# Optimization experiments

Measured on AMD Instinct MI355X. Metric: run time of the kernel, lower is better.

Reference implementation:

```python
import jax, jax.numpy as jnp
import numpy as np

N_NODES = 100000
N_EDGES = 1600000
D_IN = 128
D_H = 128          # hidden_channels * heads (heads=1)
N_LAYERS = 5
N_GRAPHS = 64
N_TARGETS = 1
EPS = 1e-5
NEG_SLOPE = 0.2    # PyG GATConv leaky_relu default


def setup_inputs() -> dict:
    key = jax.random.key(0)
    ks = jax.random.split(key, 16)
    x = jax.random.normal(ks[0], (N_NODES, D_IN), dtype=jnp.float32)
    edge_index = jax.random.randint(ks[1], (2, N_EDGES), 0, N_NODES, dtype=jnp.int32)
    batch = jnp.sort(jax.random.randint(ks[2], (N_NODES,), 0, N_GRAPHS, dtype=jnp.int32))
    s = 1.0 / np.sqrt(D_H)
    W = jax.random.normal(ks[3], (N_LAYERS, D_IN, D_H), dtype=jnp.float32) * s
    a_src = jax.random.normal(ks[4], (N_LAYERS, D_H), dtype=jnp.float32) * s
    a_dst = jax.random.normal(ks[5], (N_LAYERS, D_H), dtype=jnp.float32) * s
    b = jax.random.normal(ks[6], (N_LAYERS, D_H), dtype=jnp.float32) * 0.01
    bn_gamma = jnp.ones((N_LAYERS, D_H), dtype=jnp.float32) + 0.1 * jax.random.normal(ks[7], (N_LAYERS, D_H), dtype=jnp.float32)
    bn_beta = 0.1 * jax.random.normal(ks[8], (N_LAYERS, D_H), dtype=jnp.float32)
    bn_mean = 0.1 * jax.random.normal(ks[9], (N_LAYERS, D_H), dtype=jnp.float32)
    bn_var = jax.random.uniform(ks[10], (N_LAYERS, D_H), dtype=jnp.float32, minval=0.5, maxval=1.5)
    lin_w = jax.random.normal(ks[11], (D_H, N_TARGETS), dtype=jnp.float32) * s
    lin_b = jnp.zeros((N_TARGETS,), dtype=jnp.float32)
    return {"x": x, "edge_index": edge_index, "batch": batch, "W": W,
            "a_src": a_src, "a_dst": a_dst, "b": b,
            "bn_gamma": bn_gamma, "bn_beta": bn_beta, "bn_mean": bn_mean,
            "bn_var": bn_var, "lin_w": lin_w, "lin_b": lin_b}


def _gat_layer(h, src, dst, W, a_s, a_d, bias):
    # PyG GATConv (heads=1): linear transform, per-edge attention, softmax over
    # incoming edges of each destination node, weighted sum aggregation.
    xp = h @ W                                   # [N, C]
    s_node = xp @ a_s                            # [N]
    d_node = xp @ a_d                            # [N]
    e = jax.nn.leaky_relu(s_node[src] + d_node[dst], NEG_SLOPE)   # [E]
    m = jax.ops.segment_max(e, dst, num_segments=N_NODES)         # [N]
    w = jnp.exp(e - m[dst])                                       # [E]
    denom = jax.ops.segment_sum(w, dst, num_segments=N_NODES)     # [N] (>0: self-loops)
    alpha = w / denom[dst]                                        # [E]
    out = jax.ops.segment_sum(alpha[:, None] * xp[src], dst, num_segments=N_NODES)
    return out + bias


def reference(x, edge_index, batch, W, a_src, a_dst, b,
              bn_gamma, bn_beta, bn_mean, bn_var, lin_w, lin_b):
    # add self-loops (PyG GATConv default add_self_loops=True)
    loops = jnp.arange(N_NODES, dtype=edge_index.dtype)
    src = jnp.concatenate([edge_index[0], loops])
    dst = jnp.concatenate([edge_index[1], loops])
    h = x
    for l in range(N_LAYERS):
        h = _gat_layer(h, src, dst, W[l], a_src[l], a_dst[l], b[l])
        h = jax.nn.relu(h)
        # dropout: identity (eval mode); BatchNorm1d in eval mode (running stats)
        h = (h - bn_mean[l]) * (bn_gamma[l] / jnp.sqrt(bn_var[l] + EPS)) + bn_beta[l]
    # global mean pool over graphs
    sums = jax.ops.segment_sum(h, batch, num_segments=N_GRAPHS)            # [G, C]
    cnt = jax.ops.segment_sum(jnp.ones((N_NODES,), h.dtype), batch, num_segments=N_GRAPHS)
    g = sums / jnp.maximum(cnt, 1.0)[:, None]
    return g @ lin_w + lin_b
```

## Files before the change

### kernel.cpp

```cpp
#include <hip/hip_runtime.h>
#include <hip/hip_fp16.h>
#include <math.h>


#define NN 100000
#define NE 1600000
#define DH 128
#define NL 5
#define NG 64

static constexpr int ET = NE + NN;
static constexpr int NBK = (NN + 255) >> 8;
static constexpr int CAP = 6144;
static constexpr int GB0 = (NN + 127) / 128;
static constexpr int SBK = (ET + 4095) / 4096;
static constexpr int PW = (NL * DH * DH) / 256;
static constexpr int PB = (NL * DH + 255) / 256;
static constexpr int PC = (NN + 4095) / 4096;

typedef __attribute__((ext_vector_type(8))) _Float16 f16x8;
typedef __attribute__((ext_vector_type(4))) float f32x4;
typedef __attribute__((ext_vector_type(2))) float f32x2;

__device__ __forceinline__ unsigned short f2h(float v) {
    __half h = __float2half(v);
    return *reinterpret_cast<unsigned short*>(&h);
}
__device__ __forceinline__ float h2f(unsigned short u) {
    __half h = *reinterpret_cast<__half*>(&u);
    return __half2float(h);
}


__global__ __launch_bounds__(256) void k_prep(const float* __restrict__ W,
                                              unsigned short* __restrict__ wtg,
                                              const float* __restrict__ ga,
                                              const float* __restrict__ be,
                                              const float* __restrict__ me,
                                              const float* __restrict__ va,
                                              float* __restrict__ g2,
                                              float* __restrict__ b2,
                                              const int* __restrict__ batch,
                                              int* __restrict__ cnts) {
    __shared__ int hc[NG];
    int bid = blockIdx.x, t = threadIdx.x;
    if (bid < PW) {
        int i = bid * 256 + t;
        int l = i >> 14, rem = i & 16383;
        int k = rem >> 7, c = rem & 127;
        wtg[(l << 14) + (c << 7) + k] = f2h(W[i]);
    } else if (bid < PW + PB) {
        int i = (bid - PW) * 256 + t;
        if (i < NL * DH) {
            float s = ga[i] * rsqrtf(va[i] + 1e-5f);
            g2[i] = s;
            b2[i] = be[i] - me[i] * s;
        }
    } else {
        if (t < NG) hc[t] = 0;
        __syncthreads();
        int base = (bid - PW - PB) * 4096;
#pragma unroll
        for (int k = 0; k < 16; ++k) {
            int i = base + k * 256 + t;
            if (i < NN) atomicAdd(&hc[batch[i]], 1);
        }
        __syncthreads();
        if (t < NG && hc[t]) atomicAdd(&cnts[t], hc[t]);
    }
}


template <bool F32IN>
__device__ __forceinline__ void gemm_body(char* lds, int bid,
                                          const void* __restrict__ Av,
                                          const unsigned short* __restrict__ Wt,
                                          const float* __restrict__ a_s,
                                          const float* __restrict__ a_d,
                                          unsigned char* __restrict__ xq,
                                          float* __restrict__ s_node,
                                          float* __restrict__ d_node) {
    int tid = threadIdx.x;
    int w = tid >> 6, l = tid & 63;
    int row0 = bid * 128;
    {
        int col = tid >> 2, seg = tid & 3;
        const char* srcp = (const char*)Wt + col * 256 + seg * 64;
#pragma unroll
        for (int i = 0; i < 4; ++i) {
            int off = seg * 64 + i * 16;
            *(uint4*)(lds + col * 256 + (off ^ ((col & 7) << 4))) =
                *(const uint4*)(srcp + i * 16);
        }
    }
    int arow = row0 + w * 16 + (l & 15);
    int arc = min(arow, NN - 1);
    f16x8 af[4];
    if constexpr (F32IN) {
        const float* ap = (const float*)Av + (size_t)arc * DH + ((l >> 4) << 3);
#pragma unroll
        for (int ks = 0; ks < 4; ++ks) {
            float4 u0 = *(const float4*)(ap + ks * 32);
            float4 u1 = *(const float4*)(ap + ks * 32 + 4);
            f16x8 v = {(_Float16)u0.x, (_Float16)u0.y, (_Float16)u0.z, (_Float16)u0.w,
                       (_Float16)u1.x, (_Float16)u1.y, (_Float16)u1.z, (_Float16)u1.w};
            af[ks] = v;
        }
    } else {
        const unsigned short* ap =
            (const unsigned short*)Av + (size_t)arc * DH + ((l >> 4) << 3);
#pragma unroll
        for (int ks = 0; ks < 4; ++ks)
            af[ks] = *(const f16x8*)(ap + ks * 32);
    }
    __syncthreads();

    f32x4 acc[8];
#pragma unroll
    for (int ct = 0; ct < 8; ++ct) acc[ct] = (f32x4){0.f, 0.f, 0.f, 0.f};
#pragma unroll
    for (int ct = 0; ct < 8; ++ct) {
        int col = ct * 16 + (l & 15);
        int cb = col * 256;
        int sw = (col & 7) << 4;
#pragma unroll
        for (int ks = 0; ks < 4; ++ks) {
            f16x8 bfr = *(const f16x8*)(lds + cb + ((ks * 64 + ((l >> 4) << 4)) ^ sw));
            acc[ct] = __builtin_amdgcn_mfma_f32_16x16x32_f16(af[ks], bfr, acc[ct], 0, 0, 0);
        }
    }

    float asv[8], adv[8];
#pragma unroll
    for (int ct = 0; ct < 8; ++ct) {
        asv[ct] = a_s[ct * 16 + (l & 15)];
        adv[ct] = a_d[ct * 16 + (l & 15)];
    }
    float ps[4] = {0.f, 0.f, 0.f, 0.f}, pd[4] = {0.f, 0.f, 0.f, 0.f};
#pragma unroll
    for (int ct = 0; ct < 8; ++ct)
#pragma unroll
        for (int r = 0; r < 4; ++r) {
            ps[r] = fmaf(acc[ct][r], asv[ct], ps[r]);
            pd[r] = fmaf(acc[ct][r], adv[ct], pd[r]);
        }
#pragma unroll
    for (int off = 8; off >= 1; off >>= 1)
#pragma unroll
        for (int r = 0; r < 4; ++r) {
            ps[r] += __shfl_xor(ps[r], off, 64);
            pd[r] += __shfl_xor(pd[r], off, 64);
        }
    int rbase = row0 + w * 16 + ((l >> 4) << 2);
    if ((l & 15) == 0) {
#pragma unroll
        for (int r = 0; r < 4; ++r) {
            int row = rbase + r;
            if (row < NN) { s_node[row] = ps[r]; d_node[row] = pd[r]; }
        }
    }
#pragma unroll
    for (int r = 0; r < 4; ++r) {
        int row = rbase + r;
        if (row < NN) {
            unsigned char* op = xq + (size_t)row * DH + (l & 15);
#pragma unroll
            for (int ct = 0; ct < 8; ++ct) {
                int pk = __builtin_amdgcn_cvt_pk_fp8_f32(acc[ct][r], 0.f, 0, false);
                op[ct * 16] = (unsigned char)(pk & 0xff);
            }
        }
    }
}


__device__ __forceinline__ void bscatter_body(char* smem, int bid,
                                              const int* __restrict__ src,
                                              const int* __restrict__ dst,
                                              int* __restrict__ bcnt,
                                              int* __restrict__ pairs) {
    int* lcnt = (int*)smem;
    int* lbase = lcnt + NBK;
    for (int i = threadIdx.x; i < NBK; i += 512) lcnt[i] = 0;
    __syncthreads();
    int base = bid * 4096;
    int es[8], ed[8], er[8];
#pragma unroll
    for (int k = 0; k < 8; ++k) {
        int i = base + k * 512 + threadIdx.x;
        if (i < ET) {
            int s, d;
            if (i < NE) { s = src[i]; d = dst[i]; } else { s = d = i - NE; }
            es[k] = s; ed[k] = d;
            er[k] = atomicAdd(&lcnt[d >> 8], 1);
        } else {
            ed[k] = -1;
        }
    }
    __syncthreads();
    for (int i = threadIdx.x; i < NBK; i += 512)
        lbase[i] = lcnt[i] ? atomicAdd(&bcnt[i], lcnt[i]) : 0;
    __syncthreads();
#pragma unroll
    for (int k = 0; k < 8; ++k) {
        if (ed[k] >= 0) {
            int bk = ed[k] >> 8;
            pairs[(size_t)bk * CAP + lbase[bk] + er[k]] =
                es[k] | ((ed[k] & 255) << 17);
        }
    }
}


__global__ __launch_bounds__(512) void k_mega(const float* __restrict__ x,
                                              const unsigned short* __restrict__ Wt,
                                              const float* __restrict__ a_s,
                                              const float* __restrict__ a_d,
                                              unsigned char* __restrict__ xq,
                                              float* __restrict__ s_node,
                                              float* __restrict__ d_node,
                                              const int* __restrict__ src,
                                              const int* __restrict__ dst,
                                              int* __restrict__ bcnt,
                                              int* __restrict__ pairs) {
    __shared__ __align__(16) char smem[35904];
    if (blockIdx.x < GB0)
        gemm_body<true>(smem, blockIdx.x, x, Wt, a_s, a_d, xq, s_node, d_node);
    else
        bscatter_body(smem, blockIdx.x - GB0, src, dst, bcnt, pairs);
}


__global__ __launch_bounds__(512) void k_gemm(const unsigned short* __restrict__ A,
                                              const unsigned short* __restrict__ Wt,
                                              const float* __restrict__ a_s,
                                              const float* __restrict__ a_d,
                                              unsigned char* __restrict__ xq,
                                              float* __restrict__ s_node,
                                              float* __restrict__ d_node) {
    __shared__ __align__(16) char lds[32768];
    gemm_body<false>(lds, blockIdx.x, A, Wt, a_s, a_d, xq, s_node, d_node);
}


__global__ __launch_bounds__(512) void k_bscan(const int* __restrict__ bcnt,
                                               int* __restrict__ bbase,
                                               int* __restrict__ row_ptr) {
    __shared__ int sm[512];
    int t = threadIdx.x;
    int v = (t < NBK) ? bcnt[t] : 0;
    sm[t] = v;
    __syncthreads();
    for (int off = 1; off < 512; off <<= 1) {
        int u = (t >= off) ? sm[t - off] : 0;
        __syncthreads();
        sm[t] += u;
        __syncthreads();
    }
    if (t < NBK) bbase[t] = sm[t] - v;
    if (t == 0) { bbase[NBK] = ET; row_ptr[NN] = ET; }
}

__global__ __launch_bounds__(256) void k_bfinal(const int* __restrict__ pairs,
                                                const int* __restrict__ bcnt,
                                                const int* __restrict__ bbase,
                                                int* __restrict__ row_ptr,
                                                int* __restrict__ csr_src) {
    __shared__ int ldeg[256];
    __shared__ int lcur[256];
    __shared__ int sm[256];
    int b = blockIdx.x, t = threadIdx.x;
    int n0 = b << 8;
    int e0 = bbase[b];
    int cb = bcnt[b];
    const int* slab = pairs + (size_t)b * CAP;
    ldeg[t] = 0;
    __syncthreads();
    for (int j = t; j < cb; j += 256)
        atomicAdd(&ldeg[(slab[j] >> 17) & 255], 1);
    __syncthreads();
    int v = ldeg[t];
    sm[t] = v;
    __syncthreads();
    for (int off = 1; off < 256; off <<= 1) {
        int u = (t >= off) ? sm[t - off] : 0;
        __syncthreads();
        sm[t] += u;
        __syncthreads();
    }
    int excl = sm[t] - v;
    lcur[t] = excl;
    int n = n0 + t;
    if (n < NN) row_ptr[n] = e0 + excl;
    __syncthreads();
    for (int j = t; j < cb; j += 256) {
        int p = slab[j];
        int local = atomicAdd(&lcur[(p >> 17) & 255], 1);
        csr_src[e0 + local] = p & 0x1FFFF;
    }
}


__global__ __launch_bounds__(256) void k_aggr(const unsigned char* __restrict__ xq,
                                              const float* __restrict__ s_node,
                                              const float* __restrict__ d_node,
                                              const int* __restrict__ row_ptr,
                                              const int* __restrict__ csr_src,
                                              const float* __restrict__ bias,
                                              const float* __restrict__ g2,
                                              const float* __restrict__ b2,
                                              unsigned short* __restrict__ hout) {
    __shared__ float2 stash[4][2][64];
    int wid = threadIdx.x >> 6, lane = threadIdx.x & 63;
    int hi = lane >> 5, cl = lane & 31;
    int n = blockIdx.x * 8 + wid * 2 + hi;
    int s0 = row_ptr[n], s1 = row_ptr[n + 1];
    int deg = s1 - s0;
    float dn = d_node[n];

    int off0 = 0, off1 = 0;
    float e0 = -1e30f, e1 = -1e30f;
    {
        int j0 = s0 + cl;
        if (j0 < s1) {
            int s = csr_src[j0];
            off0 = s << 7;
            float t = s_node[s] + dn;
            e0 = (t >= 0.f) ? t : 0.2f * t;
        }
        int j1 = s0 + 32 + cl;
        if (j1 < s1) {
            int s = csr_src[j1];
            off1 = s << 7;
            float t = s_node[s] + dn;
            e1 = (t >= 0.f) ? t : 0.2f * t;
        }
    }
    float mx = fmaxf(e0, e1);
    for (int j = s0 + 64 + cl; j < s1; j += 32) {
        int s = csr_src[j];
        float t = s_node[s] + dn;
        t = (t >= 0.f) ? t : 0.2f * t;
        mx = fmaxf(mx, t);
    }
#pragma unroll
    for (int off = 16; off >= 1; off >>= 1)
        mx = fmaxf(mx, __shfl_xor(mx, off, 32));

    float w0 = (e0 > -1e29f) ? __expf(e0 - mx) : 0.f;
    float w1 = (e1 > -1e29f) ? __expf(e1 - mx) : 0.f;
    float denom = w0 + w1;
#pragma unroll
    for (int off = 16; off >= 1; off >>= 1)
        denom += __shfl_xor(denom, off, 32);

    stash[wid][hi][cl]      = make_float2(w0, __int_as_float(off0));
    stash[wid][hi][cl + 32] = make_float2(w1, __int_as_float(off1));

    unsigned int cl4 = (unsigned int)cl << 2;
    const char* xbase = (const char*)xq;
    float acc0 = 0.f, acc1 = 0.f, acc2 = 0.f, acc3 = 0.f;
    int cnt = min(deg, 64);
#pragma unroll 8
    for (int t = 0; t < cnt; ++t) {
        float2 p = stash[wid][hi][t];
        float w = p.x;
        unsigned int voff = (unsigned int)__float_as_int(p.y) + cl4;
        unsigned int v = *(const unsigned int*)(xbase + voff);
        f32x2 d0 = __builtin_amdgcn_cvt_pk_f32_fp8(v, false);
        f32x2 d1 = __builtin_amdgcn_cvt_pk_f32_fp8(v, true);
        acc0 = fmaf(w, d0[0], acc0);
        acc1 = fmaf(w, d0[1], acc1);
        acc2 = fmaf(w, d1[0], acc2);
        acc3 = fmaf(w, d1[1], acc3);
    }
    for (int j = s0 + 64; j < s1; ++j) {
        int s = csr_src[j];
        float t = s_node[s] + dn;
        t = (t >= 0.f) ? t : 0.2f * t;
        float w = __expf(t - mx);
        denom += w;
        unsigned int voff = ((unsigned int)s << 7) + cl4;
        unsigned int v = *(const unsigned int*)(xbase + voff);
        f32x2 d0 = __builtin_amdgcn_cvt_pk_f32_fp8(v, false);
        f32x2 d1 = __builtin_amdgcn_cvt_pk_f32_fp8(v, true);
        acc0 = fmaf(w, d0[0], acc0);
        acc1 = fmaf(w, d0[1], acc1);
        acc2 = fmaf(w, d1[0], acc2);
        acc3 = fmaf(w, d1[1], acc3);
    }

    float inv = 1.f / denom;
    int c = cl << 2;
    float4 bi = *(const float4*)(bias + c);
    float4 gg = *(const float4*)(g2 + c);
    float4 bb = *(const float4*)(b2 + c);
    float o0 = fmaxf(fmaf(acc0, inv, bi.x), 0.f) * gg.x + bb.x;
    float o1 = fmaxf(fmaf(acc1, inv, bi.y), 0.f) * gg.y + bb.y;
    float o2 = fmaxf(fmaf(acc2, inv, bi.z), 0.f) * gg.z + bb.z;
    float o3 = fmaxf(fmaf(acc3, inv, bi.w), 0.f) * gg.w + bb.w;
    ushort4 ov = {f2h(o0), f2h(o1), f2h(o2), f2h(o3)};
    *(ushort4*)(hout + (size_t)n * DH + c) = ov;
}


__global__ __launch_bounds__(128) void k_pool1(const unsigned short* __restrict__ h,
                                               const int* __restrict__ batch,
                                               float* __restrict__ sums) {
    int c = threadIdx.x;
    int n0 = blockIdx.x * 64;
    int n1 = min(NN, n0 + 64);
    if (n0 >= NN) return;
    float acc = 0.f;
    int cur = batch[n0];
    for (int n = n0; n < n1; ++n) {
        int g = batch[n];
        if (g != cur) {
            atomicAdd(&sums[cur * DH + c], acc);
            acc = 0.f; cur = g;
        }
        acc += h2f(h[(size_t)n * DH + c]);
    }
    atomicAdd(&sums[cur * DH + c], acc);
}

__global__ __launch_bounds__(128) void k_pool2(const float* __restrict__ sums,
                                               const int* __restrict__ cnts,
                                               const float* __restrict__ lin_w,
                                               const float* __restrict__ lin_b,
                                               float* __restrict__ out) {
    __shared__ float sm[128];
    int g = blockIdx.x, c = threadIdx.x;
    float cnt = fmaxf((float)cnts[g], 1.f);
    sm[c] = (sums[g * DH + c] / cnt) * lin_w[c];
    __syncthreads();
    for (int off = 64; off >= 1; off >>= 1) {
        if (c < off) sm[c] += sm[c + off];
        __syncthreads();
    }
    if (c == 0) out[g] = sm[0] + lin_b[0];
}


extern "C" void kernel_launch(void* const* d_in, const int* in_sizes, int n_in,
                              void* d_out, int out_size, void* d_ws, size_t ws_size,
                              hipStream_t stream) {
    const float* x     = (const float*)d_in[0];
    const int*   ei    = (const int*)d_in[1];
    const int*   batch = (const int*)d_in[2];
    const float* W     = (const float*)d_in[3];
    const float* a_src = (const float*)d_in[4];
    const float* a_dst = (const float*)d_in[5];
    const float* b     = (const float*)d_in[6];
    const float* bn_g  = (const float*)d_in[7];
    const float* bn_b  = (const float*)d_in[8];
    const float* bn_m  = (const float*)d_in[9];
    const float* bn_v  = (const float*)d_in[10];
    const float* lin_w = (const float*)d_in[11];
    const float* lin_b = (const float*)d_in[12];
    float* out = (float*)d_out;

    const int* srcp = ei;
    const int* dstp = ei + NE;

    char* wsp = (char*)d_ws;
    size_t off = 0;
    auto alloc = [&](size_t bytes) -> void* {
        void* p = wsp + off;
        off = (off + bytes + 511) & ~((size_t)511);
        return p;
    };
    unsigned char*  xq  = (unsigned char*)alloc((size_t)NN * DH);
    unsigned short* hb  = (unsigned short*)alloc((size_t)NN * DH * 2);
    unsigned short* wtg = (unsigned short*)alloc((size_t)NL * DH * DH * 2);
    float* g2      = (float*)alloc((size_t)NL * DH * 4);
    float* b2      = (float*)alloc((size_t)NL * DH * 4);
    float* s_node  = (float*)alloc((size_t)NN * 4);
    float* d_node  = (float*)alloc((size_t)NN * 4);
    int*   row_ptr = (int*)alloc((size_t)(NN + 1) * 4);
    int*   csr_src = (int*)alloc((size_t)ET * 4);
    int*   pairs   = (int*)alloc((size_t)NBK * CAP * 4);
    int*   bcnt    = (int*)alloc((size_t)NBK * 4);
    int*   bbase   = (int*)alloc((size_t)(NBK + 1) * 4);
    float* sums    = (float*)alloc((size_t)NG * DH * 4);
    int*   cnts    = (int*)alloc((size_t)NG * 4);

    hipError_t e0_ = hipMemsetAsync(bcnt, 0, (size_t)NBK * 4, stream); (void)e0_;
    hipError_t e1_ = hipMemsetAsync(sums, 0, (size_t)NG * DH * 4, stream); (void)e1_;
    hipError_t e2_ = hipMemsetAsync(cnts, 0, (size_t)NG * 4, stream); (void)e2_;

    k_prep<<<PW + PB + PC, 256, 0, stream>>>(W, wtg, bn_g, bn_b, bn_m, bn_v,
                                             g2, b2, batch, cnts);

    k_mega<<<GB0 + SBK, 512, 0, stream>>>(x, wtg, a_src, a_dst, xq,
                                          s_node, d_node, srcp, dstp, bcnt, pairs);
    k_bscan<<<1, 512, 0, stream>>>(bcnt, bbase, row_ptr);
    k_bfinal<<<NBK, 256, 0, stream>>>(pairs, bcnt, bbase, row_ptr, csr_src);

    for (int l = 0; l < NL; ++l) {
        if (l > 0)
            k_gemm<<<GB0, 512, 0, stream>>>(hb, wtg + (size_t)l * DH * DH,
                                            a_src + l * DH, a_dst + l * DH,
                                            xq, s_node, d_node);
        k_aggr<<<NN / 8, 256, 0, stream>>>(xq, s_node, d_node, row_ptr, csr_src,
                                           b + l * DH, g2 + l * DH, b2 + l * DH,
                                           hb);
    }

    k_pool1<<<(NN + 63) / 64, 128, 0, stream>>>(hb, batch, sums);
    k_pool2<<<NG, 128, 0, stream>>>(sums, cnts, lin_w, lin_b, out);
}
```

Measured before the change: 384.3 us.

## Stage fp8 GEMM output through LDS, fold bucket scan into bfinal, unroll aggregation

```diff
diff --git a/kernel.cpp b/kernel.cpp
--- a/kernel.cpp
+++ b/kernel.cpp
@@ -17,6 +17,7 @@
 static constexpr int PW = (NL * DH * DH) / 256;
 static constexpr int PB = (NL * DH + 255) / 256;
 static constexpr int PC = (NN + 4095) / 4096;
+static constexpr int LROW = 144;
 
 typedef __attribute__((ext_vector_type(8))) _Float16 f16x8;
 typedef __attribute__((ext_vector_type(4))) float f32x4;
@@ -159,16 +160,26 @@
             if (row < NN) { s_node[row] = ps[r]; d_node[row] = pd[r]; }
         }
     }
+
+    __syncthreads();
+    int rl0 = w * 16 + ((l >> 4) << 2);
 #pragma unroll
     for (int r = 0; r < 4; ++r) {
-        int row = rbase + r;
-        if (row < NN) {
-            unsigned char* op = xq + (size_t)row * DH + (l & 15);
-#pragma unroll
-            for (int ct = 0; ct < 8; ++ct) {
-                int pk = __builtin_amdgcn_cvt_pk_fp8_f32(acc[ct][r], 0.f, 0, false);
-                op[ct * 16] = (unsigned char)(pk & 0xff);
-            }
+#pragma unroll
+        for (int ct = 0; ct < 8; ++ct) {
+            int pk = __builtin_amdgcn_cvt_pk_fp8_f32(acc[ct][r], 0.f, 0, false);
+            lds[(rl0 + r) * LROW + ct * 16 + (l & 15)] = (char)(pk & 0xff);
+        }
+    }
+    __syncthreads();
+    size_t base = (size_t)row0 * DH;
+    size_t limit = (size_t)NN * DH;
+#pragma unroll
+    for (int p = 0; p < 2; ++p) {
+        int q = (tid + p * 512) * 16;
+        if (base + q < limit) {
+            int row = q >> 7, col = q & 127;
+            *(uint4*)(xq + base + q) = *(const uint4*)(lds + row * LROW + col);
         }
     }
 }
@@ -223,7 +234,7 @@
                                               const int* __restrict__ dst,
                                               int* __restrict__ bcnt,
                                               int* __restrict__ pairs) {
-    __shared__ __align__(16) char smem[35904];
+    __shared__ __align__(16) char smem[32768];
     if (blockIdx.x < GB0)
         gemm_body<true>(smem, blockIdx.x, x, Wt, a_s, a_d, xq, s_node, d_node);
     else
@@ -243,27 +254,8 @@
 }
 
 
-__global__ __launch_bounds__(512) void k_bscan(const int* __restrict__ bcnt,
-                                               int* __restrict__ bbase,
-                                               int* __restrict__ row_ptr) {
-    __shared__ int sm[512];
-    int t = threadIdx.x;
-    int v = (t < NBK) ? bcnt[t] : 0;
-    sm[t] = v;
-    __syncthreads();
-    for (int off = 1; off < 512; off <<= 1) {
-        int u = (t >= off) ? sm[t - off] : 0;
-        __syncthreads();
-        sm[t] += u;
-        __syncthreads();
-    }
-    if (t < NBK) bbase[t] = sm[t] - v;
-    if (t == 0) { bbase[NBK] = ET; row_ptr[NN] = ET; }
-}
-
 __global__ __launch_bounds__(256) void k_bfinal(const int* __restrict__ pairs,
                                                 const int* __restrict__ bcnt,
-                                                const int* __restrict__ bbase,
                                                 int* __restrict__ row_ptr,
                                                 int* __restrict__ csr_src) {
     __shared__ int ldeg[256];
@@ -271,8 +263,17 @@
     __shared__ int sm[256];
     int b = blockIdx.x, t = threadIdx.x;
     int n0 = b << 8;
-    int e0 = bbase[b];
+    int psum = 0;
+    for (int j = t; j < b; j += 256) psum += bcnt[j];
+    sm[t] = psum;
+    __syncthreads();
+    for (int off = 128; off >= 1; off >>= 1) {
+        if (t < off) sm[t] += sm[t + off];
+        __syncthreads();
+    }
+    int e0 = sm[0];
     int cb = bcnt[b];
+    __syncthreads();
     const int* slab = pairs + (size_t)b * CAP;
     ldeg[t] = 0;
     __syncthreads();
@@ -292,6 +293,7 @@
     lcur[t] = excl;
     int n = n0 + t;
     if (n < NN) row_ptr[n] = e0 + excl;
+    if (b == 0 && t == 0) row_ptr[NN] = ET;
     __syncthreads();
     for (int j = t; j < cb; j += 256) {
         int p = slab[j];
@@ -361,7 +363,7 @@
     const char* xbase = (const char*)xq;
     float acc0 = 0.f, acc1 = 0.f, acc2 = 0.f, acc3 = 0.f;
     int cnt = min(deg, 64);
-#pragma unroll 8
+#pragma unroll 16
     for (int t = 0; t < cnt; ++t) {
         float2 p = stash[wid][hi][t];
         float w = p.x;
@@ -481,7 +483,6 @@
     int*   csr_src = (int*)alloc((size_t)ET * 4);
     int*   pairs   = (int*)alloc((size_t)NBK * CAP * 4);
     int*   bcnt    = (int*)alloc((size_t)NBK * 4);
-    int*   bbase   = (int*)alloc((size_t)(NBK + 1) * 4);
     float* sums    = (float*)alloc((size_t)NG * DH * 4);
     int*   cnts    = (int*)alloc((size_t)NG * 4);
 
@@ -494,8 +495,7 @@
 
     k_mega<<<GB0 + SBK, 512, 0, stream>>>(x, wtg, a_src, a_dst, xq,
                                           s_node, d_node, srcp, dstp, bcnt, pairs);
-    k_bscan<<<1, 512, 0, stream>>>(bcnt, bbase, row_ptr);
-    k_bfinal<<<NBK, 256, 0, stream>>>(pairs, bcnt, bbase, row_ptr, csr_src);
+    k_bfinal<<<NBK, 256, 0, stream>>>(pairs, bcnt, row_ptr, csr_src);
 
     for (int l = 0; l < NL; ++l) {
         if (l > 0)
```

Result: slower. 469.6 us (+22.2%).
